# Performance work log

Hardware: AMD Instinct MI355X
Metric: run time of the kernel (lower is better)

## Reference

```python
import jax, jax.numpy as jnp
import numpy as np

B, C, W, F, NC = 512, 12, 4, 512, 4  # batch, leads, windows(=4, hardcoded by conv0), features, classes


def setup_inputs() -> dict:
    key = jax.random.key(0)
    ks = jax.random.split(key, 16)
    g = lambda i, shape, s=1.0: jax.random.normal(ks[i], shape, jnp.float32) * s
    return {
        "x": g(0, (B, C, W, F)),
        # GRU (PyTorch layout: W_ih [3F,F], W_hh [3F,F], gate order r,z,n)
        "gru_wih": g(1, (3 * F, F), 0.03),
        "gru_whh": g(2, (3 * F, F), 0.03),
        "gru_bih": jnp.zeros((3 * F,), jnp.float32),
        "gru_bhh": jnp.zeros((3 * F,), jnp.float32),
        # GraphLearning 1x1 convs (squeezed kernels); positive biases keep adj nondegenerate
        "conv0_w": g(3, (W,), 0.5), "conv0_b": jnp.float32(0.1),
        "conv1_w": g(4, (F,), 0.05), "conv1_b": jnp.float32(0.1),
        "conv2_w": g(5, (C * C, C), 0.3),
        "conv2_b": 0.1 + 0.05 * jnp.abs(g(6, (C * C,))),
        # GCN stack
        "gcn_w": g(7, (2, F, F), 0.04), "gcn_b": jnp.zeros((2, F), jnp.float32),
        # classifier head (jax [in,out] layout); BN in eval mode
        "fc1_w": g(8, (C * F, 512), 0.02), "fc1_b": jnp.zeros((512,), jnp.float32),
        "bn1_g": jnp.ones((512,), jnp.float32), "bn1_b": jnp.zeros((512,), jnp.float32),
        "bn1_m": 0.1 * g(9, (512,)), "bn1_v": 1.0 + 0.1 * jnp.abs(g(10, (512,))),
        "fc2_w": g(11, (512, 512), 0.04), "fc2_b": jnp.zeros((512,), jnp.float32),
        "bn2_g": jnp.ones((512,), jnp.float32), "bn2_b": jnp.zeros((512,), jnp.float32),
        "bn2_m": 0.1 * g(12, (512,)), "bn2_v": 1.0 + 0.1 * jnp.abs(g(13, (512,))),
        "fc3_w": g(14, (512, NC), 0.04), "fc3_b": jnp.zeros((NC,), jnp.float32),
    }


def reference(x, gru_wih, gru_whh, gru_bih, gru_bhh,
              conv0_w, conv0_b, conv1_w, conv1_b, conv2_w, conv2_b,
              gcn_w, gcn_b,
              fc1_w, fc1_b, bn1_g, bn1_b, bn1_m, bn1_v,
              fc2_w, fc2_b, bn2_g, bn2_b, bn2_m, bn2_v,
              fc3_w, fc3_b):
    b, c, w, f = x.shape
    # --- GRU over leads dim; each window slice starts from h0=0, so merge (batch, w) ---
    xs = x.transpose(0, 2, 1, 3).reshape(b * w, c, f)            # [N, C, F]
    xW = jnp.einsum('ntf,gf->ntg', xs, gru_wih) + gru_bih        # precompute input gates [N,C,3F]

    def step(h, xw_t):
        hg = h @ gru_whh.T + gru_bhh
        xr, xz, xn = jnp.split(xw_t, 3, axis=-1)
        hr, hz, hn = jnp.split(hg, 3, axis=-1)
        r = jax.nn.sigmoid(xr + hr)
        z = jax.nn.sigmoid(xz + hz)
        n = jnp.tanh(xn + r * hn)
        h = (1.0 - z) * n + z * h
        return h, h

    _, hs = jax.lax.scan(step, jnp.zeros((b * w, f), x.dtype), xW.transpose(1, 0, 2))
    gru_out = hs.transpose(1, 0, 2).reshape(b, w, c, f).transpose(0, 2, 1, 3)  # [B,C,W,F]

    # --- GraphLearning: 1x1 convs -> 12x12 adjacency -> normalized Laplacian -> Chebyshev K=4 ---
    g0 = gru_out.transpose(0, 2, 1, 3)                               # [B,W,C,F]
    y = jax.nn.relu(jnp.einsum('bwcf,w->bcf', g0, conv0_w) + conv0_b)  # [B,C,F]
    y = jax.nn.relu(jnp.einsum('bcf,f->bc', y, conv1_w) + conv1_b)     # [B,C]
    y = jax.nn.relu(jnp.einsum('bc,kc->bk', y, conv2_w) + conv2_b)     # [B,C*C]
    a = jnp.mean(y.reshape(b, c, c), axis=0)
    adj = jax.nn.relu(a)
    degree = jnp.sum(adj, axis=1)
    adj_s = 0.5 * (adj + adj.T)
    d_hat = 1.0 / (jnp.sqrt(degree) + 1e-7)
    lap = d_hat[:, None] * (jnp.diag(degree) - adj_s) * d_hat[None, :]
    L0 = jnp.zeros_like(lap)
    L1 = lap
    L2 = 2.0 * lap @ L1 - L0
    L3 = 2.0 * lap @ L2 - L1
    cheb = jnp.stack([L0, L1, L2, L3], axis=0)                       # [4,C,C]

    # --- GCN stack with residuals (dropout is identity in eval) ---
    h = gru_out.transpose(0, 2, 1, 3)[:, :, None]                    # [B,W,1,C,F]
    tmp = h
    res = h
    for i in range(gcn_w.shape[0]):
        support = jnp.einsum('bwocf,fg->bwocg', h, gcn_w[i])
        out = jnp.einsum('wij,bwojf->bwoif', cheb, support) + gcn_b[i]
        h = jax.nn.relu(out) + res
        res = h
    h = tmp + h
    h = h[:, :, 0].sum(1).reshape(b, c * f)                          # [B, C*F]

    # --- classifier head (eval-mode BN, dropout identity) ---
    def bn(v, gmm, bt, m, var):
        return (v - m) / jnp.sqrt(var + 1e-5) * gmm + bt

    h = bn(jax.nn.leaky_relu(h @ fc1_w + fc1_b, 0.01), bn1_g, bn1_b, bn1_m, bn1_v)
    h = bn(jax.nn.leaky_relu(h @ fc2_w + fc2_b, 0.01), bn2_g, bn2_b, bn2_m, bn2_v)
    return h @ fc3_w + fc3_b
```

## Files before the change

### kernel.cpp

```cpp
#include <hip/hip_runtime.h>
#include <cmath>

constexpr int Bb  = 512;
constexpr int Cc  = 12;
constexpr int Ww  = 4;
constexpr int Ff  = 512;
constexpr int Mx  = Bb * Ww * Cc;

typedef __attribute__((ext_vector_type(8))) short bf16x8;
typedef __attribute__((ext_vector_type(4))) float f32x4;

__device__ __forceinline__ float sigm(float v) { return 1.f / (1.f + expf(-v)); }
__device__ __forceinline__ float b2f(ushort u) { union { float f; unsigned i; } v; v.i = ((unsigned)u) << 16; return v.f; }
__device__ __forceinline__ ushort f2b(float f) {
    union { float f; unsigned i; } v; v.f = f;
    unsigned r = v.i + 0x7FFFu + ((v.i >> 16) & 1u);
    return (ushort)(r >> 16);
}
__device__ __forceinline__ float fsigm(float v) {
    return __builtin_amdgcn_rcpf(1.f + __builtin_amdgcn_exp2f(v * -1.44269504f));
}
__device__ __forceinline__ float ftanh(float v) {
    return 1.f - 2.f * __builtin_amdgcn_rcpf(1.f + __builtin_amdgcn_exp2f(v * 2.88539008f));
}
__device__ __forceinline__ void async16(const ushort* g, ushort* l) {
    __builtin_amdgcn_global_load_lds(
        (const __attribute__((address_space(1))) unsigned int*)g,
        (__attribute__((address_space(3))) unsigned int*)l, 16, 0, 0);
}

__global__ __launch_bounds__(256) void mfma_gemm(
    const ushort* __restrict__ A, const ushort* __restrict__ Bt,
    float* __restrict__ Cf, ushort* __restrict__ Cb,
    const float* __restrict__ colBias,
    int N, int K, int kLen, int MN, int gridY)
{
    __shared__ ushort As[128 * 64], Bs[128 * 64];
    const int tid = threadIdx.x;
    const int ln = tid & 63, wv = tid >> 6;
    const int l = blockIdx.x;
    const int by = l % gridY, bx = l / gridY, bz = blockIdx.y;
    const int srow = ln >> 3;
    const int kslot = (ln & 7) ^ srow;
    const int rowA0 = by * 128 + wv * 32;
    const int rowB0 = bx * 128 + wv * 32;
    const ushort* ga = A  + (long)(rowA0 + srow) * K + bz * kLen + kslot * 8;
    const ushort* gb = Bt + (long)(rowB0 + srow) * K + bz * kLen + kslot * 8;
    ushort* la = As + wv * 32 * 64;
    ushort* lb = Bs + wv * 32 * 64;
    const int rbase = (wv >> 1) * 64, cbase = (wv & 1) * 64;
    const int mrow = ln & 15, quad = ln >> 4;

    f32x4 acc[4][4] = {};

    for (int kc = 0; kc < kLen; kc += 64) {
        #pragma unroll
        for (int i = 0; i < 4; ++i) {
            async16(ga + (long)(i * 8) * K, la + i * 8 * 64);
            async16(gb + (long)(i * 8) * K, lb + i * 8 * 64);
        }
        ga += 64; gb += 64;
        __syncthreads();
        #pragma unroll
        for (int s = 0; s < 2; ++s) {
            const int sw = (((s << 2) + quad) ^ (ln & 7)) << 3;
            bf16x8 af[4], bf[4];
            #pragma unroll
            for (int i = 0; i < 4; ++i)
                af[i] = *(const bf16x8*)(As + (rbase + i * 16 + mrow) * 64 + sw);
            #pragma unroll
            for (int j = 0; j < 4; ++j)
                bf[j] = *(const bf16x8*)(Bs + (cbase + j * 16 + mrow) * 64 + sw);
            #pragma unroll
            for (int i = 0; i < 4; ++i)
                #pragma unroll
                for (int j = 0; j < 4; ++j)
                    acc[i][j] = __builtin_amdgcn_mfma_f32_16x16x32_bf16(bf[j], af[i], acc[i][j], 0, 0, 0);
        }
        __syncthreads();
    }

    const int gr0 = by * 128 + rbase + mrow;
    const int gc0 = bx * 128 + cbase + quad * 4;
    if (Cb) {
        #pragma unroll
        for (int i = 0; i < 4; ++i) {
            const long rowoff = (long)(gr0 + i * 16) * N;
            #pragma unroll
            for (int j = 0; j < 4; ++j) {
                float c0 = 0.f, c1 = 0.f, c2 = 0.f, c3 = 0.f;
                if (colBias) {
                    const float4 cb4 = *(const float4*)(colBias + gc0 + j * 16);
                    c0 = cb4.x; c1 = cb4.y; c2 = cb4.z; c3 = cb4.w;
                }
                union { ushort u[4]; uint2 v; } pk;
                pk.u[0] = f2b(acc[i][j][0] + c0);
                pk.u[1] = f2b(acc[i][j][1] + c1);
                pk.u[2] = f2b(acc[i][j][2] + c2);
                pk.u[3] = f2b(acc[i][j][3] + c3);
                *(uint2*)&Cb[rowoff + gc0 + j * 16] = pk.v;
            }
        }
    } else {
        float* Co = Cf + (long)bz * MN;
        #pragma unroll
        for (int i = 0; i < 4; ++i) {
            const long rowoff = (long)(gr0 + i * 16) * N;
            #pragma unroll
            for (int j = 0; j < 4; ++j)
                *(f32x4*)&Co[rowoff + gc0 + j * 16] = acc[i][j];
        }
    }
}

__global__ __launch_bounds__(512, 1) void gru_persist(
    const ushort* __restrict__ xW, const ushort* __restrict__ whhB,
    const float* __restrict__ bih, const float* __restrict__ bhh,
    ushort* __restrict__ h0, ushort* __restrict__ h1,
    ushort* __restrict__ G, unsigned* __restrict__ bar)
{
    __shared__ ushort Bw[8 * 96 * 64];
    const int tid = threadIdx.x, ln = tid & 63, wv = tid >> 6;
    const int mb = blockIdx.x & 15, fb = blockIdx.x >> 4;
    const int srow = ln >> 3, kslot = (ln & 7) ^ srow;
    const int mrow = ln & 15, quad = ln >> 4;

    #pragma unroll
    for (int i = 0; i < 12; ++i) {
        const int rg = i * 8 + wv;
        const int kc6 = rg / 12, rgi = rg - kc6 * 12;
        const int r0 = rgi * 8, r = r0 + srow;
        const int g = r >> 5, fc = r & 31;
        async16(whhB + (long)(g * 512 + fb * 32 + fc) * 512 + kc6 * 64 + kslot * 8,
                Bw + (kc6 * 96 + r0) * 64);
    }

    float br[2][4], bz[2][4], bni[2][4], bnh[2][4];
    #pragma unroll
    for (int ft = 0; ft < 2; ++ft) {
        const int f0 = fb * 32 + ft * 16 + quad * 4;
        const float4 bir = *(const float4*)(bih + f0);
        const float4 biz = *(const float4*)(bih + 512 + f0);
        const float4 bin = *(const float4*)(bih + 1024 + f0);
        const float4 bhr = *(const float4*)(bhh + f0);
        const float4 bhz = *(const float4*)(bhh + 512 + f0);
        const float4 bhn = *(const float4*)(bhh + 1024 + f0);
        br[ft][0] = bir.x + bhr.x; br[ft][1] = bir.y + bhr.y; br[ft][2] = bir.z + bhr.z; br[ft][3] = bir.w + bhr.w;
        bz[ft][0] = biz.x + bhz.x; bz[ft][1] = biz.y + bhz.y; bz[ft][2] = biz.z + bhz.z; bz[ft][3] = biz.w + bhz.w;
        bni[ft][0] = bin.x; bni[ft][1] = bin.y; bni[ft][2] = bin.z; bni[ft][3] = bin.w;
        bnh[ft][0] = bhn.x; bnh[ft][1] = bhn.y; bnh[ft][2] = bhn.z; bnh[ft][3] = bhn.w;
    }
    __syncthreads();

    const int n = mb * 128 + wv * 16 + mrow;
    unsigned* cptr = bar + mb * 16;

    const int rbase0 = ((mb * 8 + wv) * 16) * 512;
    const int aoff = (quad >> 1) * 256 + mrow * 16 + (quad & 1) * 8;
    const int sbase = ((mb * 8 + wv) * 16 + fb) * 512 + mrow * 16 + quad * 4;

    uint2 hprev[2]; hprev[0].x = 0u; hprev[0].y = 0u; hprev[1] = hprev[0];

    for (int t = 0; t < 12; ++t) {
        const ushort* hin = (t & 1) ? h1 : h0;
        ushort* hout = (t & 1) ? h0 : h1;
        f32x4 acc[6] = {};

        unsigned long long ha[16][2];
        if (t > 0) {
            #pragma unroll
            for (int sl = 0; sl < 16; ++sl) {
                const ushort* p = hin + rbase0 + sl * 512 + aoff;
                ha[sl][0] = __hip_atomic_load((const unsigned long long*)p,
                                              __ATOMIC_RELAXED, __HIP_MEMORY_SCOPE_AGENT);
                ha[sl][1] = __hip_atomic_load((const unsigned long long*)(p + 4),
                                              __ATOMIC_RELAXED, __HIP_MEMORY_SCOPE_AGENT);
            }
        }

        const long xrow = ((long)n * 12 + t) * 1536;
        uint2 xrv[2], xzv[2], xnv[2];
        #pragma unroll
        for (int ft = 0; ft < 2; ++ft) {
            const int f0 = fb * 32 + ft * 16 + quad * 4;
            xrv[ft] = *(const uint2*)(xW + xrow + f0);
            xzv[ft] = *(const uint2*)(xW + xrow + 512 + f0);
            xnv[ft] = *(const uint2*)(xW + xrow + 1024 + f0);
        }

        if (t > 0) {
            #pragma unroll
            for (int kc = 0; kc < 8; ++kc) {
                const ushort* Bk = Bw + kc * (96 * 64);
                #pragma unroll
                for (int s = 0; s < 2; ++s) {
                    union { unsigned long long q[2]; bf16x8 v; } af;
                    af.q[0] = ha[kc * 2 + s][0];
                    af.q[1] = ha[kc * 2 + s][1];
                    const int sw = (((s << 2) + quad) ^ (ln & 7)) << 3;
                    #pragma unroll
                    for (int jt = 0; jt < 6; ++jt) {
                        const bf16x8 bh = *(const bf16x8*)(Bk + (jt * 16 + mrow) * 64 + sw);
                        acc[jt] = __builtin_amdgcn_mfma_f32_16x16x32_bf16(bh, af.v, acc[jt], 0, 0, 0);
                    }
                }
            }
        }

        #pragma unroll
        for (int ft = 0; ft < 2; ++ft) {
            const ushort* xr = (const ushort*)&xrv[ft];
            const ushort* xz = (const ushort*)&xzv[ft];
            const ushort* xn = (const ushort*)&xnv[ft];
            const ushort* hp = (const ushort*)&hprev[ft];
            union { ushort u[4]; uint2 v; } o;
            #pragma unroll
            for (int r = 0; r < 4; ++r) {
                const float rr = fsigm(acc[ft][r] + b2f(xr[r]) + br[ft][r]);
                const float zz = fsigm(acc[2 + ft][r] + b2f(xz[r]) + bz[ft][r]);
                const float nv = ftanh(b2f(xn[r]) + bni[ft][r] + rr * (acc[4 + ft][r] + bnh[ft][r]));
                o.u[r] = f2b((1.f - zz) * nv + zz * b2f(hp[r]));
            }
            hprev[ft] = o.v;
        }

        if (t < 11) {
            union { uint2 v; unsigned long long q; } q0, q1;
            q0.v = hprev[0]; q1.v = hprev[1];
            __hip_atomic_store((unsigned long long*)&hout[sbase], q0.q,
                               __ATOMIC_RELAXED, __HIP_MEMORY_SCOPE_AGENT);
            __hip_atomic_store((unsigned long long*)&hout[sbase + 256], q1.q,
                               __ATOMIC_RELAXED, __HIP_MEMORY_SCOPE_AGENT);
            asm volatile("s_waitcnt vmcnt(0)" ::: "memory");
            __syncthreads();
            if (tid == 0)
                __hip_atomic_fetch_add(cptr, 1u, __ATOMIC_RELAXED, __HIP_MEMORY_SCOPE_AGENT);
        }

        {
            const int f0 = fb * 32 + quad * 4;
            *(uint2*)&G[((long)n * 12 + t) * 512 + f0] = hprev[0];
            *(uint2*)&G[((long)n * 12 + t) * 512 + f0 + 16] = hprev[1];
        }

        if (t < 11) {
            if (tid == 0) {
                const unsigned tgt = (unsigned)(t + 1) * 16u;
                while (__hip_atomic_load(cptr, __ATOMIC_RELAXED, __HIP_MEMORY_SCOPE_AGENT) < tgt)
                    __builtin_amdgcn_s_sleep(1);
            }
            __syncthreads();
        }
    }
}

__global__ __launch_bounds__(256) void cvt_x(const float* __restrict__ x, ushort* __restrict__ xb)
{
    const int idx = blockIdx.x * 256 + threadIdx.x;
    const int m = idx >> 6, f8 = (idx & 63) << 3;
    const int n = m / 12, c = m - n * 12;
    const int b = n >> 2, w = n & 3;
    const float* src = x + (((b * 12 + c) * 4 + w) << 9) + f8;
    const float4 a = *(const float4*)src, q = *(const float4*)(src + 4);
    uint4 o;
    o.x = (unsigned)f2b(a.x) | ((unsigned)f2b(a.y) << 16);
    o.y = (unsigned)f2b(a.z) | ((unsigned)f2b(a.w) << 16);
    o.z = (unsigned)f2b(q.x) | ((unsigned)f2b(q.y) << 16);
    o.w = (unsigned)f2b(q.z) | ((unsigned)f2b(q.w) << 16);
    *(uint4*)(xb + (m << 9) + f8) = o;
}

__global__ __launch_bounds__(256) void cvt_w2(
    const float* __restrict__ wih, const float* __restrict__ whh,
    ushort* __restrict__ wihB, ushort* __restrict__ whhB)
{
    int bx = blockIdx.x;
    const float* s; ushort* d;
    if (bx < 384) { s = wih; d = wihB; } else { s = whh; d = whhB; bx -= 384; }
    const int e = (bx * 256 + threadIdx.x) << 3;
    const float4 a = *(const float4*)(s + e), q = *(const float4*)(s + e + 4);
    uint4 o;
    o.x = (unsigned)f2b(a.x) | ((unsigned)f2b(a.y) << 16);
    o.y = (unsigned)f2b(a.z) | ((unsigned)f2b(a.w) << 16);
    o.z = (unsigned)f2b(q.x) | ((unsigned)f2b(q.y) << 16);
    o.w = (unsigned)f2b(q.z) | ((unsigned)f2b(q.w) << 16);
    *(uint4*)(d + e) = o;
}

__global__ __launch_bounds__(256) void tcvt_all(
    const float* __restrict__ gcnw, const float* __restrict__ f1w, const float* __restrict__ f2w,
    ushort* __restrict__ gw0, ushort* __restrict__ gw1,
    ushort* __restrict__ f1t, ushort* __restrict__ f2t)
{
    int by = blockIdx.y;
    const float* src; ushort* dst; int R, C;
    if (by < 16)       { src = gcnw;          dst = gw0; R = 512;  C = 512; }
    else if (by < 32)  { src = gcnw + 262144; dst = gw1; R = 512;  C = 512; by -= 16; }
    else if (by < 224) { src = f1w;           dst = f1t; R = 6144; C = 512; by -= 32; }
    else               { src = f2w;           dst = f2t; R = 512;  C = 512; by -= 224; }
    __shared__ float tl[32][33];
    const int c0 = blockIdx.x * 32, r0 = by * 32;
    const int cx = threadIdx.x & 31, ry = threadIdx.x >> 5;
    #pragma unroll
    for (int k = 0; k < 4; ++k) tl[ry + k * 8][cx] = src[(long)(r0 + ry + k * 8) * C + c0 + cx];
    __syncthreads();
    #pragma unroll
    for (int k = 0; k < 4; ++k) dst[(long)(c0 + ry + k * 8) * R + r0 + cx] = f2b(tl[cx][ry + k * 8]);
}

__global__ __launch_bounds__(256) void conv01(
    const ushort* __restrict__ G, const float* __restrict__ w0, const float* __restrict__ b0,
    const float* __restrict__ w1, const float* __restrict__ b1, float* __restrict__ y2)
{
    const int row = (blockIdx.x * 256 + threadIdx.x) >> 6;
    const int lane = threadIdx.x & 63;
    const int b = row / 12, c = row - 12 * b;
    const float w00 = w0[0], w01 = w0[1], w02 = w0[2], w03 = w0[3], bb = b0[0];
    const ushort* gp = G + ((long)(b * 4) * 12 + c) * 512;
    float s = 0.f;
    for (int f = lane; f < 512; f += 64) {
        const float v = bb + b2f(gp[f]) * w00 + b2f(gp[6144 + f]) * w01
                      + b2f(gp[12288 + f]) * w02 + b2f(gp[18432 + f]) * w03;
        s += fmaxf(v, 0.f) * w1[f];
    }
    #pragma unroll
    for (int off = 32; off; off >>= 1) s += __shfl_down(s, off);
    if (lane == 0) y2[row] = fmaxf(s + b1[0], 0.f);
}

__global__ __launch_bounds__(256) void conv2_cheb(
    const float* __restrict__ y2, const float* __restrict__ w2,
    const float* __restrict__ b2, float* __restrict__ cheb)
{
    __shared__ float ys[6144];
    __shared__ float adj[144], deg[12], dhat[12], lap[144], T2[144];
    const int tid = threadIdx.x;
    for (int i = tid; i < 6144; i += 256) ys[i] = y2[i];
    __syncthreads();
    if (tid < 144) {
        float wk[12];
        #pragma unroll
        for (int c = 0; c < 12; ++c) wk[c] = w2[tid * 12 + c];
        const float bias = b2[tid];
        float s = 0.f;
        for (int b = 0; b < 512; ++b) {
            float v = bias;
            #pragma unroll
            for (int c = 0; c < 12; ++c) v += ys[b * 12 + c] * wk[c];
            s += fmaxf(v, 0.f);
        }
        adj[tid] = fmaxf(s * (1.f / 512.f), 0.f);
    }
    __syncthreads();
    if (tid < 12) {
        float s = 0.f;
        for (int j = 0; j < 12; ++j) s += adj[tid * 12 + j];
        deg[tid] = s; dhat[tid] = 1.f / (sqrtf(s) + 1e-7f);
    }
    __syncthreads();
    if (tid < 144) {
        const int i = tid / 12, j = tid % 12;
        const float as = 0.5f * (adj[i * 12 + j] + adj[j * 12 + i]);
        lap[tid] = dhat[i] * ((i == j ? deg[i] : 0.f) - as) * dhat[j];
    }
    __syncthreads();
    if (tid < 144) {
        const int i = tid / 12, j = tid % 12;
        float s = 0.f;
        for (int kk = 0; kk < 12; ++kk) s += lap[i * 12 + kk] * lap[kk * 12 + j];
        T2[tid] = 2.f * s;
    }
    __syncthreads();
    if (tid < 144) {
        const int i = tid / 12, j = tid % 12;
        float s = 0.f;
        for (int kk = 0; kk < 12; ++kk) s += lap[i * 12 + kk] * T2[kk * 12 + j];
        cheb[tid] = 0.f;
        cheb[144 + tid] = lap[tid];
        cheb[288 + tid] = T2[tid];
        cheb[432 + tid] = 2.f * s - lap[tid];
    }
}

__global__ __launch_bounds__(256) void gcn_epi1(
    const ushort* __restrict__ S, const float* __restrict__ cheb,
    const float* __restrict__ gcnb, const ushort* __restrict__ G,
    ushort* __restrict__ H1)
{
    __shared__ float ch[576];
    const int tid = threadIdx.x;
    for (int i = tid; i < 576; i += 256) ch[i] = cheb[i];
    __syncthreads();
    const int idx = blockIdx.x * 256 + tid;
    const int f = idx & 511, bc = idx >> 9;
    const int b = bc / 12, c = bc - 12 * b;
    const float bias = gcnb[f];
    #pragma unroll
    for (int w = 0; w < 4; ++w) {
        float o = bias;
        const ushort* Sr = S + ((b * 4 + w) * 12) * 512 + f;
        const float* cw = ch + w * 144 + c * 12;
        #pragma unroll
        for (int j = 0; j < 12; ++j) o += cw[j] * b2f(Sr[j * 512]);
        const int gi = ((b * 4 + w) * 12 + c) * 512 + f;
        H1[gi] = f2b(fmaxf(o, 0.f) + b2f(G[gi]));
    }
}

__global__ __launch_bounds__(256) void gcn_epi2(
    const ushort* __restrict__ S, const float* __restrict__ cheb,
    const float* __restrict__ gcnb, const ushort* __restrict__ G,
    const ushort* __restrict__ H1, ushort* __restrict__ pooled)
{
    __shared__ float ch[576];
    const int tid = threadIdx.x;
    for (int i = tid; i < 576; i += 256) ch[i] = cheb[i];
    __syncthreads();
    const int idx = blockIdx.x * 256 + tid;
    const int f = idx & 511, bc = idx >> 9;
    const int b = bc / 12, c = bc - 12 * b;
    const float bias = gcnb[f];
    float acc = 0.f;
    #pragma unroll
    for (int w = 0; w < 4; ++w) {
        float o = bias;
        const ushort* Sr = S + ((b * 4 + w) * 12) * 512 + f;
        const float* cw = ch + w * 144 + c * 12;
        #pragma unroll
        for (int j = 0; j < 12; ++j) o += cw[j] * b2f(Sr[j * 512]);
        const int gi = ((b * 4 + w) * 12 + c) * 512 + f;
        acc += fmaxf(o, 0.f) + b2f(H1[gi]) + b2f(G[gi]);
    }
    pooled[idx] = f2b(acc);
}

__global__ __launch_bounds__(256) void fc_epi(
    const float* __restrict__ part, int nsplit, const float* __restrict__ bias,
    const float* __restrict__ g, const float* __restrict__ be,
    const float* __restrict__ mu, const float* __restrict__ var,
    ushort* __restrict__ outb, float* __restrict__ outf)
{
    const int idx = blockIdx.x * 256 + threadIdx.x;
    const int c = idx & 511;
    float s = bias[c];
    for (int k = 0; k < nsplit; ++k) s += part[k * 262144 + idx];
    s = s >= 0.f ? s : 0.01f * s;
    s = (s - mu[c]) * rsqrtf(var[c] + 1e-5f) * g[c] + be[c];
    if (outb) outb[idx] = f2b(s); else outf[idx] = s;
}

__global__ __launch_bounds__(256) void fc3_kernel(
    const float* __restrict__ z2, const float* __restrict__ w3,
    const float* __restrict__ b3, float* __restrict__ out)
{
    const int idx = blockIdx.x * 256 + threadIdx.x;
    const int m = idx >> 2, nc = idx & 3;
    float s = b3[nc];
    const float* zr = z2 + m * 512;
    for (int k = 0; k < 512; ++k) s += zr[k] * w3[k * 4 + nc];
    out[idx] = s;
}

extern "C" void kernel_launch(void* const* d_in, const int* in_sizes, int n_in,
                              void* d_out, int out_size, void* d_ws, size_t ws_size,
                              hipStream_t stream)
{
    (void)in_sizes; (void)n_in; (void)out_size; (void)ws_size;
    const float* x    = (const float*)d_in[0];
    const float* wih  = (const float*)d_in[1];
    const float* whh  = (const float*)d_in[2];
    const float* bih  = (const float*)d_in[3];
    const float* bhh  = (const float*)d_in[4];
    const float* c0w  = (const float*)d_in[5];
    const float* c0b  = (const float*)d_in[6];
    const float* c1w  = (const float*)d_in[7];
    const float* c1b  = (const float*)d_in[8];
    const float* c2w  = (const float*)d_in[9];
    const float* c2b  = (const float*)d_in[10];
    const float* gcnw = (const float*)d_in[11];
    const float* gcnb = (const float*)d_in[12];
    const float* f1w  = (const float*)d_in[13];
    const float* f1b  = (const float*)d_in[14];
    const float* bn1g = (const float*)d_in[15];
    const float* bn1b = (const float*)d_in[16];
    const float* bn1m = (const float*)d_in[17];
    const float* bn1v = (const float*)d_in[18];
    const float* f2w  = (const float*)d_in[19];
    const float* f2b_ = (const float*)d_in[20];
    const float* bn2g = (const float*)d_in[21];
    const float* bn2b = (const float*)d_in[22];
    const float* bn2m = (const float*)d_in[23];
    const float* bn2v = (const float*)d_in[24];
    const float* f3w  = (const float*)d_in[25];
    const float* f3b  = (const float*)d_in[26];

    char* W = (char*)d_ws;
    ushort* xW     = (ushort*)(W + 0);
    ushort* S      = (ushort*)(W + 0);
    ushort* H1     = (ushort*)(W + 25165824);
    ushort* pooled = (ushort*)(W + 50331648);
    float*  z1p    = (float*)(W + 58720256);
    float*  z2p    = z1p;
    ushort* xb     = (ushort*)(W + 75497472);
    ushort* G      = (ushort*)(W + 75497472);
    ushort* h0     = (ushort*)(W + 100663296);
    ushort* h1     = (ushort*)(W + 102760448);
    ushort* whhB   = (ushort*)(W + 104857600);
    ushort* wihB   = (ushort*)(W + 106430464);
    ushort* gw0    = (ushort*)(W + 108003328);
    ushort* gw1    = (ushort*)(W + 108527616);
    ushort* f1t    = (ushort*)(W + 109051904);
    ushort* f2t    = (ushort*)(W + 115343360);
    ushort* z1b    = (ushort*)(W + 115867648);
    float*  z2     = (float*)(W + 116391936);
    float*  y2     = (float*)(W + 117440512);
    float*  chebb  = (float*)(W + 117465088);
    unsigned* bar  = (unsigned*)(W + 117467392);

    hipMemsetAsync(bar, 0, 1024, stream);
    cvt_x<<<(Mx * 64) / 256, 256, 0, stream>>>(x, xb);
    cvt_w2<<<768, 256, 0, stream>>>(wih, whh, wihB, whhB);
    tcvt_all<<<dim3(16, 240), 256, 0, stream>>>(gcnw, f1w, f2w, gw0, gw1, f1t, f2t);

    mfma_gemm<<<dim3(2304, 1), 256, 0, stream>>>(
        xb, wihB, nullptr, xW, nullptr, 3 * Ff, Ff, Ff, 0, 192);
    gru_persist<<<256, 512, 0, stream>>>(xW, whhB, bih, bhh, h0, h1, G, bar);

    conv01<<<(Bb * Cc * 64) / 256, 256, 0, stream>>>(G, c0w, c0b, c1w, c1b, y2);
    conv2_cheb<<<1, 256, 0, stream>>>(y2, c2w, c2b, chebb);

    mfma_gemm<<<dim3(768, 1), 256, 0, stream>>>(
        G, gw0, nullptr, S, nullptr, Ff, Ff, Ff, 0, 192);
    gcn_epi1<<<(Bb * Cc * Ff) / 256, 256, 0, stream>>>(S, chebb, gcnb, G, H1);

    mfma_gemm<<<dim3(768, 1), 256, 0, stream>>>(
        H1, gw1, nullptr, S, nullptr, Ff, Ff, Ff, 0, 192);
    gcn_epi2<<<(Bb * Cc * Ff) / 256, 256, 0, stream>>>(S, chebb, gcnb + Ff, G, H1, pooled);

    mfma_gemm<<<dim3(16, 16), 256, 0, stream>>>(
        pooled, f1t, z1p, nullptr, nullptr, 512, Cc * Ff, 384, 262144, 4);
    fc_epi<<<1024, 256, 0, stream>>>(z1p, 16, f1b, bn1g, bn1b, bn1m, bn1v, z1b, nullptr);
    mfma_gemm<<<dim3(16, 4), 256, 0, stream>>>(
        z1b, f2t, z2p, nullptr, nullptr, 512, 512, 128, 262144, 4);
    fc_epi<<<1024, 256, 0, stream>>>(z2p, 4, f2b_, bn2g, bn2b, bn2m, bn2v, nullptr, z2);
    fc3_kernel<<<(Bb * 4) / 256, 256, 0, stream>>>(z2, f3w, f3b, (float*)d_out);
}
```

Baseline: 475.7 us.

## Remap GRU waves to 2 row tiles by 1 column half for B-fragment reuse

```diff
diff --git a/kernel.cpp b/kernel.cpp
--- a/kernel.cpp
+++ b/kernel.cpp
@@ -124,68 +124,75 @@
     const int mb = blockIdx.x & 15, fb = blockIdx.x >> 4;
     const int srow = ln >> 3, kslot = (ln & 7) ^ srow;
     const int mrow = ln & 15, quad = ln >> 4;
+    const int rg = wv >> 1, cg = wv & 1;
 
     #pragma unroll
     for (int i = 0; i < 12; ++i) {
-        const int rg = i * 8 + wv;
-        const int kc6 = rg / 12, rgi = rg - kc6 * 12;
+        const int rgx = i * 8 + wv;
+        const int kc6 = rgx / 12, rgi = rgx - kc6 * 12;
         const int r0 = rgi * 8, r = r0 + srow;
         const int g = r >> 5, fc = r & 31;
         async16(whhB + (long)(g * 512 + fb * 32 + fc) * 512 + kc6 * 64 + kslot * 8,
                 Bw + (kc6 * 96 + r0) * 64);
     }
 
-    float br[2][4], bz[2][4], bni[2][4], bnh[2][4];
-    #pragma unroll
-    for (int ft = 0; ft < 2; ++ft) {
-        const int f0 = fb * 32 + ft * 16 + quad * 4;
+    const int f0 = fb * 32 + cg * 16 + quad * 4;
+    float br[4], bz[4], bni[4], bnh[4];
+    {
         const float4 bir = *(const float4*)(bih + f0);
         const float4 biz = *(const float4*)(bih + 512 + f0);
         const float4 bin = *(const float4*)(bih + 1024 + f0);
         const float4 bhr = *(const float4*)(bhh + f0);
         const float4 bhz = *(const float4*)(bhh + 512 + f0);
         const float4 bhn = *(const float4*)(bhh + 1024 + f0);
-        br[ft][0] = bir.x + bhr.x; br[ft][1] = bir.y + bhr.y; br[ft][2] = bir.z + bhr.z; br[ft][3] = bir.w + bhr.w;
-        bz[ft][0] = biz.x + bhz.x; bz[ft][1] = biz.y + bhz.y; bz[ft][2] = biz.z + bhz.z; bz[ft][3] = biz.w + bhz.w;
-        bni[ft][0] = bin.x; bni[ft][1] = bin.y; bni[ft][2] = bin.z; bni[ft][3] = bin.w;
-        bnh[ft][0] = bhn.x; bnh[ft][1] = bhn.y; bnh[ft][2] = bhn.z; bnh[ft][3] = bhn.w;
-    }
-    __syncthreads();
-
-    const int n = mb * 128 + wv * 16 + mrow;
+        br[0] = bir.x + bhr.x; br[1] = bir.y + bhr.y; br[2] = bir.z + bhr.z; br[3] = bir.w + bhr.w;
+        bz[0] = biz.x + bhz.x; bz[1] = biz.y + bhz.y; bz[2] = biz.z + bhz.z; bz[3] = biz.w + bhz.w;
+        bni[0] = bin.x; bni[1] = bin.y; bni[2] = bin.z; bni[3] = bin.w;
+        bnh[0] = bhn.x; bnh[1] = bhn.y; bnh[2] = bhn.z; bnh[3] = bhn.w;
+    }
+    __syncthreads();
+
+    const int n0 = mb * 128 + (rg * 2 + 0) * 16 + mrow;
+    const int n1 = n0 + 16;
     unsigned* cptr = bar + mb * 16;
 
-    const int rbase0 = ((mb * 8 + wv) * 16) * 512;
     const int aoff = (quad >> 1) * 256 + mrow * 16 + (quad & 1) * 8;
-    const int sbase = ((mb * 8 + wv) * 16 + fb) * 512 + mrow * 16 + quad * 4;
+    const long rb0 = ((long)(mb * 8 + rg * 2 + 0) * 16) * 512;
+    const long rb1 = ((long)(mb * 8 + rg * 2 + 1) * 16) * 512;
+    const int sb0 = ((mb * 8 + rg * 2 + 0) * 16 + fb) * 512 + cg * 256 + mrow * 16 + quad * 4;
+    const int sb1 = ((mb * 8 + rg * 2 + 1) * 16 + fb) * 512 + cg * 256 + mrow * 16 + quad * 4;
 
     uint2 hprev[2]; hprev[0].x = 0u; hprev[0].y = 0u; hprev[1] = hprev[0];
 
     for (int t = 0; t < 12; ++t) {
         const ushort* hin = (t & 1) ? h1 : h0;
         ushort* hout = (t & 1) ? h0 : h1;
-        f32x4 acc[6] = {};
-
-        unsigned long long ha[16][2];
+        f32x4 acc[2][3] = {};
+
+        unsigned long long ha[2][16][2];
         if (t > 0) {
             #pragma unroll
             for (int sl = 0; sl < 16; ++sl) {
-                const ushort* p = hin + rbase0 + sl * 512 + aoff;
-                ha[sl][0] = __hip_atomic_load((const unsigned long long*)p,
-                                              __ATOMIC_RELAXED, __HIP_MEMORY_SCOPE_AGENT);
-                ha[sl][1] = __hip_atomic_load((const unsigned long long*)(p + 4),
-                                              __ATOMIC_RELAXED, __HIP_MEMORY_SCOPE_AGENT);
+                const ushort* p0 = hin + rb0 + sl * 512 + aoff;
+                const ushort* p1 = hin + rb1 + sl * 512 + aoff;
+                ha[0][sl][0] = __hip_atomic_load((const unsigned long long*)p0,
+                                                 __ATOMIC_RELAXED, __HIP_MEMORY_SCOPE_AGENT);
+                ha[0][sl][1] = __hip_atomic_load((const unsigned long long*)(p0 + 4),
+                                                 __ATOMIC_RELAXED, __HIP_MEMORY_SCOPE_AGENT);
+                ha[1][sl][0] = __hip_atomic_load((const unsigned long long*)p1,
+                                                 __ATOMIC_RELAXED, __HIP_MEMORY_SCOPE_AGENT);
+                ha[1][sl][1] = __hip_atomic_load((const unsigned long long*)(p1 + 4),
+                                                 __ATOMIC_RELAXED, __HIP_MEMORY_SCOPE_AGENT);
             }
         }
 
-        const long xrow = ((long)n * 12 + t) * 1536;
         uint2 xrv[2], xzv[2], xnv[2];
         #pragma unroll
-        for (int ft = 0; ft < 2; ++ft) {
-            const int f0 = fb * 32 + ft * 16 + quad * 4;
-            xrv[ft] = *(const uint2*)(xW + xrow + f0);
-            xzv[ft] = *(const uint2*)(xW + xrow + 512 + f0);
-            xnv[ft] = *(const uint2*)(xW + xrow + 1024 + f0);
+        for (int rt = 0; rt < 2; ++rt) {
+            const long xrow = ((long)(rt ? n1 : n0) * 12 + t) * 1536;
+            xrv[rt] = *(const uint2*)(xW + xrow + f0);
+            xzv[rt] = *(const uint2*)(xW + xrow + 512 + f0);
+            xnv[rt] = *(const uint2*)(xW + xrow + 1024 + f0);
         }
 
         if (t > 0) {
@@ -194,42 +201,44 @@
                 const ushort* Bk = Bw + kc * (96 * 64);
                 #pragma unroll
                 for (int s = 0; s < 2; ++s) {
-                    union { unsigned long long q[2]; bf16x8 v; } af;
-                    af.q[0] = ha[kc * 2 + s][0];
-                    af.q[1] = ha[kc * 2 + s][1];
+                    union { unsigned long long q[2]; bf16x8 v; } a0, a1;
+                    a0.q[0] = ha[0][kc * 2 + s][0]; a0.q[1] = ha[0][kc * 2 + s][1];
+                    a1.q[0] = ha[1][kc * 2 + s][0]; a1.q[1] = ha[1][kc * 2 + s][1];
                     const int sw = (((s << 2) + quad) ^ (ln & 7)) << 3;
                     #pragma unroll
-                    for (int jt = 0; jt < 6; ++jt) {
+                    for (int g = 0; g < 3; ++g) {
+                        const int jt = g * 2 + cg;
                         const bf16x8 bh = *(const bf16x8*)(Bk + (jt * 16 + mrow) * 64 + sw);
-                        acc[jt] = __builtin_amdgcn_mfma_f32_16x16x32_bf16(bh, af.v, acc[jt], 0, 0, 0);
+                        acc[0][g] = __builtin_amdgcn_mfma_f32_16x16x32_bf16(bh, a0.v, acc[0][g], 0, 0, 0);
+                        acc[1][g] = __builtin_amdgcn_mfma_f32_16x16x32_bf16(bh, a1.v, acc[1][g], 0, 0, 0);
                     }
                 }
             }
         }
 
         #pragma unroll
-        for (int ft = 0; ft < 2; ++ft) {
-            const ushort* xr = (const ushort*)&xrv[ft];
-            const ushort* xz = (const ushort*)&xzv[ft];
-            const ushort* xn = (const ushort*)&xnv[ft];
-            const ushort* hp = (const ushort*)&hprev[ft];
+        for (int rt = 0; rt < 2; ++rt) {
+            const ushort* xr = (const ushort*)&xrv[rt];
+            const ushort* xz = (const ushort*)&xzv[rt];
+            const ushort* xn = (const ushort*)&xnv[rt];
+            const ushort* hp = (const ushort*)&hprev[rt];
             union { ushort u[4]; uint2 v; } o;
             #pragma unroll
             for (int r = 0; r < 4; ++r) {
-                const float rr = fsigm(acc[ft][r] + b2f(xr[r]) + br[ft][r]);
-                const float zz = fsigm(acc[2 + ft][r] + b2f(xz[r]) + bz[ft][r]);
-                const float nv = ftanh(b2f(xn[r]) + bni[ft][r] + rr * (acc[4 + ft][r] + bnh[ft][r]));
+                const float rr = fsigm(acc[rt][0][r] + b2f(xr[r]) + br[r]);
+                const float zz = fsigm(acc[rt][1][r] + b2f(xz[r]) + bz[r]);
+                const float nv = ftanh(b2f(xn[r]) + bni[r] + rr * (acc[rt][2][r] + bnh[r]));
                 o.u[r] = f2b((1.f - zz) * nv + zz * b2f(hp[r]));
             }
-            hprev[ft] = o.v;
+            hprev[rt] = o.v;
         }
 
         if (t < 11) {
             union { uint2 v; unsigned long long q; } q0, q1;
             q0.v = hprev[0]; q1.v = hprev[1];
-            __hip_atomic_store((unsigned long long*)&hout[sbase], q0.q,
+            __hip_atomic_store((unsigned long long*)&hout[sb0], q0.q,
                                __ATOMIC_RELAXED, __HIP_MEMORY_SCOPE_AGENT);
-            __hip_atomic_store((unsigned long long*)&hout[sbase + 256], q1.q,
+            __hip_atomic_store((unsigned long long*)&hout[sb1], q1.q,
                                __ATOMIC_RELAXED, __HIP_MEMORY_SCOPE_AGENT);
             asm volatile("s_waitcnt vmcnt(0)" ::: "memory");
             __syncthreads();
@@ -237,11 +246,8 @@
                 __hip_atomic_fetch_add(cptr, 1u, __ATOMIC_RELAXED, __HIP_MEMORY_SCOPE_AGENT);
         }
 
-        {
-            const int f0 = fb * 32 + quad * 4;
-            *(uint2*)&G[((long)n * 12 + t) * 512 + f0] = hprev[0];
-            *(uint2*)&G[((long)n * 12 + t) * 512 + f0 + 16] = hprev[1];
-        }
+        *(uint2*)&G[((long)n0 * 12 + t) * 512 + f0] = hprev[0];
+        *(uint2*)&G[((long)n1 * 12 + t) * 512 + f0] = hprev[1];
 
         if (t < 11) {
             if (tid == 0) {
```

Measured after the change: 481.8 us. Within noise of the previous version (+1.3%).
